# Kernel tuning notes

Measured on AMD Instinct MI355X. Metric: run time of the kernel, lower is better.

The kernel has to match this reference:

```python
import jax, jax.numpy as jnp
import numpy as np

K = 3
PAD = (K - 1) // 2


def _conv1d(x, w, b):
    # x: [B, T, C]; w: [F, C, K] (torch OIH layout); conv over T, 'same' padding
    y = jax.lax.conv_general_dilated(x.transpose(0, 2, 1), w, (1,), [(PAD, PAD)],
                                     dimension_numbers=('NCH', 'OIH', 'NCH'))
    return (y + b[None, :, None]).transpose(0, 2, 1)


def _ln(x, g, b, eps=1e-5):
    m = x.mean(-1, keepdims=True)
    v = ((x - m) ** 2).mean(-1, keepdims=True)
    return (x - m) * jax.lax.rsqrt(v + eps) * g + b


def _predictor(x, p):
    # Conv1d -> ReLU -> LN -> Conv1d -> ReLU -> LN -> Linear(F,1) -> ReLU -> squeeze
    w1, b1, g1, be1, w2, b2, g2, be2, wl, bl = p
    h = _ln(jax.nn.relu(_conv1d(x, w1, b1)), g1, be1)
    h = _ln(jax.nn.relu(_conv1d(h, w2, b2)), g2, be2)
    return jax.nn.relu(jnp.einsum('btf,f->bt', h, wl) + bl)  # [B, T]


def _length_regulate(x, dur, max_len):
    # Gather-based frame expansion: frame t comes from token i = searchsorted(cumsum(dur), t, 'right')
    cs = jnp.cumsum(dur, axis=1)                       # [B, T]
    t = jnp.arange(max_len)                            # [M]
    idx = jax.vmap(lambda c: jnp.searchsorted(c, t, side='right'))(cs)  # [B, M]
    valid = t[None, :] < cs[:, -1:]                    # [B, M]
    idx = jnp.minimum(idx, x.shape[1] - 1)
    out = jnp.take_along_axis(x, idx[:, :, None], axis=1)  # [B, M, C]
    out = jnp.where(valid[:, :, None], out, jnp.zeros((), x.dtype))
    mel_len = jnp.minimum(cs[:, -1], max_len)
    return out, mel_len


def _bucketize(x, boundaries):
    # torch.bucketize(right=False): first boundary > x  ==  searchsorted(side='right')
    return jnp.searchsorted(boundaries, x, side='right')


def setup_inputs() -> dict:
    key = jax.random.key(0)
    ks = jax.random.split(key, 12)
    B, T, M, C, F, NB = 32, 256, 2048, 256, 256, 256
    inp = {}
    inp['inputs'] = jax.random.normal(ks[0], (B, T, C), jnp.float32)
    inp['true_duration'] = jax.random.randint(ks[1], (B, T), 0, 16)
    inp['true_pitch'] = jax.random.uniform(ks[2], (B, M), jnp.float32) * 300.0
    inp['true_energy'] = jax.random.uniform(ks[3], (B, M), jnp.float32) * 200.0
    inp['mel_max_len'] = M
    inp['pitch_q'] = jnp.linspace(0.0, 300.0, NB - 1)
    inp['energy_q'] = jnp.linspace(0.0, 200.0, NB - 1)

    def pred_params(k, cin):
        kk = jax.random.split(k, 3)
        return [0.02 * jax.random.normal(kk[0], (F, cin, K)), jnp.zeros((F,)),
                jnp.ones((F,)), jnp.zeros((F,)),
                0.02 * jax.random.normal(kk[1], (F, F, K)), jnp.zeros((F,)),
                jnp.ones((F,)), jnp.zeros((F,)),
                0.02 * jax.random.normal(kk[2], (F,)), jnp.zeros(())]

    names = ['w1', 'b1', 'g1', 'be1', 'w2', 'b2', 'g2', 'be2', 'wl', 'bl']
    for i, pre in enumerate(['dp', 'pp', 'ep']):
        for n, v in zip(names, pred_params(ks[4 + i], C)):
            inp[pre + '_' + n] = v
    inp['pitch_emb'] = 0.02 * jax.random.normal(ks[8], (NB, C))
    inp['energy_emb'] = 0.02 * jax.random.normal(ks[9], (NB, C))
    return inp


def reference(inputs, true_duration, true_pitch, true_energy, mel_max_len,
              pitch_q, energy_q,
              dp_w1, dp_b1, dp_g1, dp_be1, dp_w2, dp_b2, dp_g2, dp_be2, dp_wl, dp_bl,
              pp_w1, pp_b1, pp_g1, pp_be1, pp_w2, pp_b2, pp_g2, pp_be2, pp_wl, pp_bl,
              ep_w1, ep_b1, ep_g1, ep_be1, ep_w2, ep_b2, ep_g2, ep_be2, ep_wl, ep_bl,
              pitch_emb, energy_emb):
    # Training path: expansion uses true_duration, embeddings use true pitch/energy.
    dp = (dp_w1, dp_b1, dp_g1, dp_be1, dp_w2, dp_b2, dp_g2, dp_be2, dp_wl, dp_bl)
    pp = (pp_w1, pp_b1, pp_g1, pp_be1, pp_w2, pp_b2, pp_g2, pp_be2, pp_wl, pp_bl)
    ep = (ep_w1, ep_b1, ep_g1, ep_be1, ep_w2, ep_b2, ep_g2, ep_be2, ep_wl, ep_bl)
    durations = _predictor(inputs, dp)                       # [B, T], alpha=1.0
    outputs, mel_len = _length_regulate(inputs, true_duration, mel_max_len)  # [B, M, C]
    pitches = _predictor(outputs, pp)                        # [B, M]
    outputs = outputs + pitch_emb[_bucketize(true_pitch, pitch_q)]
    energies = _predictor(outputs, ep)                       # [B, M]
    outputs = outputs + energy_emb[_bucketize(true_energy, energy_q)]
    return outputs, durations, pitches, energies, mel_len
```

## Files before the change

### kernel.cpp

```cpp
#include <hip/hip_runtime.h>
#include <hip/hip_bf16.h>
#include <stdint.h>

#define DUR_OFF 16777216
#define PIT_OFF 16785408
#define ENE_OFF 16850944
#define MEL_OFF 16916480

typedef __attribute__((ext_vector_type(8))) short short8;
typedef __attribute__((ext_vector_type(4))) float f32x4;

__device__ __forceinline__ void async16(const void* g, void* l) {
  __builtin_amdgcn_global_load_lds((__attribute__((address_space(1))) void*)g,
                                   (__attribute__((address_space(3))) void*)l, 16, 0, 0);
}

__device__ __forceinline__ unsigned short bfu(float f) {
  __hip_bfloat16 h = __float2bfloat16(f);
  return __builtin_bit_cast(unsigned short, h);
}
__device__ __forceinline__ float f_from_bf(unsigned short u) {
  return __builtin_bit_cast(float, (unsigned)u << 16);
}

__global__ void zero2_kernel(__hip_bfloat16* __restrict__ xb, __hip_bfloat16* __restrict__ h1,
                             __hip_bfloat16* __restrict__ M1, __hip_bfloat16* __restrict__ M2) {
  int buf = blockIdx.x >> 6, sub = blockIdx.x & 63;
  int b = sub >> 1, top = sub & 1;
  __hip_bfloat16* p; int L;
  if (buf == 0) { p = xb; L = 256; }
  else if (buf == 1) { p = h1; L = 256; }
  else if (buf == 2) { p = M1; L = 2048; }
  else { p = M2; L = 2048; }
  size_t row = (size_t)b * (L + 2) + (top ? (L + 1) : 0);
  p[row * 256 + threadIdx.x] = __float2bfloat16(0.0f);
}

__global__ void packfrag_kernel(const float* __restrict__ w0, const float* __restrict__ w1,
                                const float* __restrict__ w2, const float* __restrict__ w3,
                                const float* __restrict__ w4, const float* __restrict__ w5,
                                __hip_bfloat16* __restrict__ wpbase) {
  int t = blockIdx.x * 256 + threadIdx.x;
  int wsel = t / 24576;
  int rem = t % 24576;
  const float* w = wsel == 0 ? w0 : wsel == 1 ? w1 : wsel == 2 ? w2
                 : wsel == 3 ? w3 : wsel == 4 ? w4 : w5;
  __hip_bfloat16* wp = wpbase + (size_t)wsel * 196608;
  int L = rem & 63;
  int ks = (rem >> 6) & 7;
  int q = rem >> 9;
  int tap = q % 3, r = q / 3;
  int ni = r & 3, fb = r >> 2;
  int f = fb * 64 + ni * 16 + (L & 15);
  int cb = ks * 32 + ((L >> 4) << 3);
  short8 o;
#pragma unroll
  for (int e = 0; e < 8; ++e)
    o[e] = (short)bfu(w[((size_t)f * 256 + cb + e) * 3 + tap]);
  *(short8*)(wp + (size_t)rem * 8) = o;
}

__global__ void cvt_pad_kernel(const float* __restrict__ x, __hip_bfloat16* __restrict__ xb) {
  int idx = blockIdx.x * 256 + threadIdx.x;
  float4 v = ((const float4*)x)[idx];
  int c4 = idx & 63;
  int rowi = idx >> 6;
  int b = rowi >> 8, t = rowi & 255;
  ushort4 o;
  o.x = bfu(v.x); o.y = bfu(v.y); o.z = bfu(v.z); o.w = bfu(v.w);
  ((ushort4*)(xb + ((size_t)b * 258 + t + 1) * 256))[c4] = o;
}

__global__ void gather_kernel(const __hip_bfloat16* __restrict__ xb, const int* __restrict__ dur,
                              __hip_bfloat16* __restrict__ outB, float* __restrict__ mel) {
  __shared__ int scs[256];
  __shared__ int sidx[64];
  __shared__ int sval[64];
  int bch = blockIdx.x >> 5;
  int m0 = (blockIdx.x & 31) << 6;
  int tid = threadIdx.x;
  scs[tid] = dur[bch * 256 + tid];
  __syncthreads();
  for (int off = 1; off < 256; off <<= 1) {
    int add = (tid >= off) ? scs[tid - off] : 0;
    __syncthreads();
    scs[tid] += add;
    __syncthreads();
  }
  int total = scs[255];
  if (tid == 0 && (blockIdx.x & 31) == 0)
    mel[bch] = (float)(total < 2048 ? total : 2048);
  if (tid < 64) {
    int m = m0 + tid;
    int lo = 0, hi = 256;
    while (lo < hi) { int mid = (lo + hi) >> 1; if (scs[mid] <= m) lo = mid + 1; else hi = mid; }
    sidx[tid] = lo < 255 ? lo : 255;
    sval[tid] = (m < total);
  }
  __syncthreads();
  int lane = tid & 63, rs = tid >> 6;
  for (int r = rs; r < 64; r += 4) {
    ushort4 o = make_ushort4(0, 0, 0, 0);
    if (sval[r])
      o = ((const ushort4*)(xb + ((size_t)bch * 258 + sidx[r] + 1) * 256))[lane];
    ((ushort4*)(outB + ((size_t)bch * 2050 + m0 + r + 1) * 256))[lane] = o;
  }
}

__global__ void addemb_kernel(const float* __restrict__ tp, const float* __restrict__ te,
                              const float* __restrict__ pq, const float* __restrict__ eq,
                              const float* __restrict__ pemb, const float* __restrict__ eemb,
                              const __hip_bfloat16* __restrict__ M1, __hip_bfloat16* __restrict__ M2,
                              float* __restrict__ out) {
  __shared__ float sp[255], se[255];
  __shared__ int sip[64], sie[64];
  int bch = blockIdx.x >> 5;
  int m0 = (blockIdx.x & 31) << 6;
  int tid = threadIdx.x;
  if (tid < 255) { sp[tid] = pq[tid]; se[tid] = eq[tid]; }
  __syncthreads();
  if (tid < 64) {
    float xv = tp[bch * 2048 + m0 + tid];
    int lo = 0, hi = 255;
    while (lo < hi) { int mid = (lo + hi) >> 1; if (sp[mid] <= xv) lo = mid + 1; else hi = mid; }
    sip[tid] = lo;
    float ev = te[bch * 2048 + m0 + tid];
    lo = 0; hi = 255;
    while (lo < hi) { int mid = (lo + hi) >> 1; if (se[mid] <= ev) lo = mid + 1; else hi = mid; }
    sie[tid] = lo;
  }
  __syncthreads();
  int lane = tid & 63, rs = tid >> 6;
  for (int r = rs; r < 64; r += 4) {
    ushort4 mv = ((const ushort4*)(M1 + ((size_t)bch * 2050 + m0 + r + 1) * 256))[lane];
    float4 ep = ((const float4*)(pemb + (size_t)sip[r] * 256))[lane];
    float4 ee = ((const float4*)(eemb + (size_t)sie[r] * 256))[lane];
    float4 v;
    v.x = f_from_bf(mv.x) + ep.x; v.y = f_from_bf(mv.y) + ep.y;
    v.z = f_from_bf(mv.z) + ep.z; v.w = f_from_bf(mv.w) + ep.w;
    ushort4 o;
    o.x = bfu(v.x); o.y = bfu(v.y); o.z = bfu(v.z); o.w = bfu(v.w);
    ((ushort4*)(M2 + ((size_t)bch * 2050 + m0 + r + 1) * 256))[lane] = o;
    float4 w;
    w.x = v.x + ee.x; w.y = v.y + ee.y; w.z = v.z + ee.z; w.w = v.w + ee.w;
    ((float4*)(out + ((size_t)bch * 2048 + m0 + r) * 256))[lane] = w;
  }
}

__device__ __forceinline__ void loadB4(const char* Wb, int s, short8 (&dst)[4]) {
  int tap = s >> 3, ks = s & 7;
#pragma unroll
  for (int ni = 0; ni < 4; ++ni)
    dst[ni] = *(const short8*)(Wb + ((((ni * 3 + tap) << 3) + ks) << 10));
}

template <int MI>
__device__ __forceinline__ void sliceMFMA(int s, const char* lA, int rlane, int colp,
                                          const short8 (&bv)[4], f32x4 (&acc)[MI][4]) {
  const int tap = s >> 3, ks = s & 7;
  const int xorv = ((tap + rlane) & 7) << 4;
  short8 av[MI];
#pragma unroll
  for (int mi = 0; mi < MI; ++mi) {
    int a = (tap + (mi << 4) + rlane) * 512 + (ks << 6) + colp;
    av[mi] = *(const short8*)(lA + (a ^ xorv));
  }
#pragma unroll
  for (int mi = 0; mi < MI; ++mi)
#pragma unroll
    for (int ni = 0; ni < 4; ++ni)
      acc[mi][ni] = __builtin_amdgcn_mfma_f32_16x16x32_bf16(av[mi], bv[ni], acc[mi][ni], 0, 0, 0);
}

template <int EPI, int TM>
__global__ __launch_bounds__(256, 3)
void pred_gemm(const __hip_bfloat16* __restrict__ Ap, const __hip_bfloat16* __restrict__ Wf,
               const float* __restrict__ bias, const float* __restrict__ gamma,
               const float* __restrict__ beta, const float* __restrict__ wl,
               const float* __restrict__ blp, __hip_bfloat16* __restrict__ Hout,
               float* __restrict__ Sout, int L) {
  constexpr int MI = TM / 16;
  constexpr int ABYTES = (TM + 2) * 512;
  __shared__ char lA[ABYTES];
  __shared__ float lred[TM * 8];
  __shared__ float lstat[TM * 2];

  const int tid = threadIdx.x;
  const int wid = tid >> 6;
  const int lane = tid & 63;
  const int wn = wid;
  const int tiles = L / TM;
  const int b = blockIdx.x / tiles;
  const int t0 = (blockIdx.x % tiles) * TM;

  const char* Asrc = (const char*)(Ap + ((size_t)b * (L + 2) + t0) * 256);
#pragma unroll
  for (int j = 0; j < (ABYTES + 4095) / 4096; ++j) {
    int off = j * 4096 + tid * 16;
    if (off < ABYTES) {
      int so = off ^ (((off >> 9) & 7) << 4);
      async16(Asrc + so, lA + off);
    }
  }

  const char* Wb = (const char*)Wf + (size_t)wn * 98304 + lane * 16;

  f32x4 acc[MI][4];
  const f32x4 zero4 = {0.f, 0.f, 0.f, 0.f};
#pragma unroll
  for (int i = 0; i < MI; ++i)
#pragma unroll
    for (int j = 0; j < 4; ++j) acc[i][j] = zero4;

  short8 pA[4], pB[4];
  loadB4(Wb, 0, pA);

  __syncthreads();

  const int rlane = lane & 15;
  const int colp = (lane >> 4) << 4;
#pragma unroll 1
  for (int s2 = 0; s2 < 12; ++s2) {
    loadB4(Wb, 2 * s2 + 1, pB);
    sliceMFMA<MI>(2 * s2, lA, rlane, colp, pA, acc);
    if (s2 < 11) loadB4(Wb, 2 * s2 + 2, pA);
    sliceMFMA<MI>(2 * s2 + 1, lA, rlane, colp, pB, acc);
  }

  const int cb0 = (wn << 6) + rlane;
  float bi[4], gg[4], bb[4];
#pragma unroll
  for (int ni = 0; ni < 4; ++ni) {
    int col = cb0 + (ni << 4);
    bi[ni] = bias[col]; gg[ni] = gamma[col]; bb[ni] = beta[col];
  }
  const int rbase = (lane >> 4) << 2;
#pragma unroll
  for (int mi = 0; mi < MI; ++mi) {
#pragma unroll
    for (int j = 0; j < 4; ++j) {
      float s = 0.f, s2 = 0.f;
#pragma unroll
      for (int ni = 0; ni < 4; ++ni) {
        float r = fmaxf(acc[mi][ni][j] + bi[ni], 0.f);
        s += r; s2 += r * r;
      }
#pragma unroll
      for (int d = 1; d < 16; d <<= 1) { s += __shfl_xor(s, d); s2 += __shfl_xor(s2, d); }
      if ((lane & 15) == 0) {
        int row = (mi << 4) + rbase + j;
        lred[row * 8 + wn] = s;
        lred[row * 8 + 4 + wn] = s2;
      }
    }
  }
  __syncthreads();
  if (tid < TM) {
    float s = lred[tid * 8] + lred[tid * 8 + 1] + lred[tid * 8 + 2] + lred[tid * 8 + 3];
    float s2 = lred[tid * 8 + 4] + lred[tid * 8 + 5] + lred[tid * 8 + 6] + lred[tid * 8 + 7];
    float mean = s * (1.f / 256.f);
    float var = fmaxf(s2 * (1.f / 256.f) - mean * mean, 0.f);
    lstat[tid * 2] = mean;
    lstat[tid * 2 + 1] = rsqrtf(var + 1e-5f);
  }
  __syncthreads();

  if constexpr (EPI == 0) {
#pragma unroll
    for (int mi = 0; mi < MI; ++mi) {
#pragma unroll
      for (int j = 0; j < 4; ++j) {
        int row = (mi << 4) + rbase + j;
        float mean = lstat[row * 2], rstd = lstat[row * 2 + 1];
        __hip_bfloat16* hp = Hout + ((size_t)b * (L + 2) + t0 + row + 1) * 256 + cb0;
#pragma unroll
        for (int ni = 0; ni < 4; ++ni) {
          float r = fmaxf(acc[mi][ni][j] + bi[ni], 0.f);
          hp[ni << 4] = __float2bfloat16((r - mean) * rstd * gg[ni] + bb[ni]);
        }
      }
    }
  } else {
    float wlv[4];
#pragma unroll
    for (int ni = 0; ni < 4; ++ni) wlv[ni] = wl[cb0 + (ni << 4)];
#pragma unroll
    for (int mi = 0; mi < MI; ++mi) {
#pragma unroll
      for (int j = 0; j < 4; ++j) {
        int row = (mi << 4) + rbase + j;
        float mean = lstat[row * 2], rstd = lstat[row * 2 + 1];
        float ds = 0.f;
#pragma unroll
        for (int ni = 0; ni < 4; ++ni) {
          float r = fmaxf(acc[mi][ni][j] + bi[ni], 0.f);
          ds += ((r - mean) * rstd * gg[ni] + bb[ni]) * wlv[ni];
        }
#pragma unroll
        for (int d = 1; d < 16; d <<= 1) ds += __shfl_xor(ds, d);
        if ((lane & 15) == 0) lred[row * 8 + wn] = ds;
      }
    }
    __syncthreads();
    if (tid < TM) {
      float z = lred[tid * 8] + lred[tid * 8 + 1] + lred[tid * 8 + 2] + lred[tid * 8 + 3] + blp[0];
      Sout[(size_t)b * L + t0 + tid] = fmaxf(z, 0.f);
    }
  }
}

extern "C" void kernel_launch(void* const* d_in, const int* in_sizes, int n_in,
                              void* d_out, int out_size, void* d_ws, size_t ws_size,
                              hipStream_t stream) {
  const float* x = (const float*)d_in[0];
  const int* dur = (const int*)d_in[1];
  const float* tp = (const float*)d_in[2];
  const float* te = (const float*)d_in[3];
  const float* pq = (const float*)d_in[5];
  const float* eq = (const float*)d_in[6];
  const float* pemb = (const float*)d_in[37];
  const float* eemb = (const float*)d_in[38];

  char* ws = (char*)d_ws;
  __hip_bfloat16* wpb = (__hip_bfloat16*)ws;
  __hip_bfloat16* wp[6];
  for (int i = 0; i < 6; ++i) wp[i] = wpb + (size_t)i * 196608;
  __hip_bfloat16* xb = (__hip_bfloat16*)(ws + 2359296);
  __hip_bfloat16* h1dp = (__hip_bfloat16*)(ws + 6586368);
  __hip_bfloat16* M1 = (__hip_bfloat16*)(ws + 10813440);
  __hip_bfloat16* M2 = (__hip_bfloat16*)(ws + 44400640);

  float* out = (float*)d_out;

  zero2_kernel<<<256, 256, 0, stream>>>(xb, h1dp, M1, M2);
  packfrag_kernel<<<576, 256, 0, stream>>>((const float*)d_in[7], (const float*)d_in[11],
                                           (const float*)d_in[17], (const float*)d_in[21],
                                           (const float*)d_in[27], (const float*)d_in[31], wpb);
  cvt_pad_kernel<<<2048, 256, 0, stream>>>(x, xb);

  pred_gemm<0, 32><<<256, 256, 0, stream>>>(xb, wp[0], (const float*)d_in[8],
                                            (const float*)d_in[9], (const float*)d_in[10],
                                            nullptr, nullptr, h1dp, nullptr, 256);
  pred_gemm<1, 32><<<256, 256, 0, stream>>>(h1dp, wp[1], (const float*)d_in[12],
                                            (const float*)d_in[13], (const float*)d_in[14],
                                            (const float*)d_in[15], (const float*)d_in[16],
                                            nullptr, out + DUR_OFF, 256);

  gather_kernel<<<1024, 256, 0, stream>>>(xb, dur, M1, out + MEL_OFF);

  pred_gemm<0, 64><<<1024, 256, 0, stream>>>(M1, wp[2], (const float*)d_in[18],
                                             (const float*)d_in[19], (const float*)d_in[20],
                                             nullptr, nullptr, M2, nullptr, 2048);
  pred_gemm<1, 64><<<1024, 256, 0, stream>>>(M2, wp[3], (const float*)d_in[22],
                                             (const float*)d_in[23], (const float*)d_in[24],
                                             (const float*)d_in[25], (const float*)d_in[26],
                                             nullptr, out + PIT_OFF, 2048);

  addemb_kernel<<<1024, 256, 0, stream>>>(tp, te, pq, eq, pemb, eemb, M1, M2, out);

  pred_gemm<0, 64><<<1024, 256, 0, stream>>>(M2, wp[4], (const float*)d_in[28],
                                             (const float*)d_in[29], (const float*)d_in[30],
                                             nullptr, nullptr, M1, nullptr, 2048);
  pred_gemm<1, 64><<<1024, 256, 0, stream>>>(M1, wp[5], (const float*)d_in[32],
                                             (const float*)d_in[33], (const float*)d_in[34],
                                             (const float*)d_in[35], (const float*)d_in[36],
                                             nullptr, out + ENE_OFF, 2048);
}
```

Baseline: 348.2 us.

## Fuse both predictor conv layers into one kernel with halo recompute in LDS

Replaces the two-kernel conv1 and conv2 predictor pipeline with a single kernel. It loads an 82-row input tile, computes the first conv, ReLU and LayerNorm on 66 needed rows (padded to 80), and writes that bf16 intermediate back into shared memory. The second conv then runs from LDS, so the hidden activation no longer round-trips through global memory and one launch per predictor is removed. The cost is about 25% extra first-layer MFMA work for the halo rows, more LDS per block, loss of the B-fragment double buffering, and fewer blocks for the short duration predictor.

```diff
diff --git a/kernel.cpp b/kernel.cpp
--- a/kernel.cpp
+++ b/kernel.cpp
@@ -23,14 +23,13 @@
   return __builtin_bit_cast(float, (unsigned)u << 16);
 }
 
-__global__ void zero2_kernel(__hip_bfloat16* __restrict__ xb, __hip_bfloat16* __restrict__ h1,
-                             __hip_bfloat16* __restrict__ M1, __hip_bfloat16* __restrict__ M2) {
+__global__ void zero2_kernel(__hip_bfloat16* __restrict__ xb, __hip_bfloat16* __restrict__ M1,
+                             __hip_bfloat16* __restrict__ M2) {
   int buf = blockIdx.x >> 6, sub = blockIdx.x & 63;
   int b = sub >> 1, top = sub & 1;
   __hip_bfloat16* p; int L;
   if (buf == 0) { p = xb; L = 256; }
-  else if (buf == 1) { p = h1; L = 256; }
-  else if (buf == 2) { p = M1; L = 2048; }
+  else if (buf == 1) { p = M1; L = 2048; }
   else { p = M2; L = 2048; }
   size_t row = (size_t)b * (L + 2) + (top ? (L + 1) : 0);
   p[row * 256 + threadIdx.x] = __float2bfloat16(0.0f);
@@ -154,108 +153,100 @@
     dst[ni] = *(const short8*)(Wb + ((((ni * 3 + tap) << 3) + ks) << 10));
 }
 
-template <int MI>
-__device__ __forceinline__ void sliceMFMA(int s, const char* lA, int rlane, int colp,
-                                          const short8 (&bv)[4], f32x4 (&acc)[MI][4]) {
-  const int tap = s >> 3, ks = s & 7;
-  const int xorv = ((tap + rlane) & 7) << 4;
-  short8 av[MI];
-#pragma unroll
-  for (int mi = 0; mi < MI; ++mi) {
-    int a = (tap + (mi << 4) + rlane) * 512 + (ks << 6) + colp;
-    av[mi] = *(const short8*)(lA + (a ^ xorv));
-  }
-#pragma unroll
-  for (int mi = 0; mi < MI; ++mi)
-#pragma unroll
-    for (int ni = 0; ni < 4; ++ni)
-      acc[mi][ni] = __builtin_amdgcn_mfma_f32_16x16x32_bf16(av[mi], bv[ni], acc[mi][ni], 0, 0, 0);
-}
-
-template <int EPI, int TM>
 __global__ __launch_bounds__(256, 3)
-void pred_gemm(const __hip_bfloat16* __restrict__ Ap, const __hip_bfloat16* __restrict__ Wf,
-               const float* __restrict__ bias, const float* __restrict__ gamma,
-               const float* __restrict__ beta, const float* __restrict__ wl,
-               const float* __restrict__ blp, __hip_bfloat16* __restrict__ Hout,
-               float* __restrict__ Sout, int L) {
-  constexpr int MI = TM / 16;
-  constexpr int ABYTES = (TM + 2) * 512;
-  __shared__ char lA[ABYTES];
-  __shared__ float lred[TM * 8];
-  __shared__ float lstat[TM * 2];
+void fused_pred(const __hip_bfloat16* __restrict__ Ap, const __hip_bfloat16* __restrict__ Wf1,
+                const __hip_bfloat16* __restrict__ Wf2,
+                const float* __restrict__ b1, const float* __restrict__ g1,
+                const float* __restrict__ be1,
+                const float* __restrict__ b2, const float* __restrict__ g2,
+                const float* __restrict__ be2,
+                const float* __restrict__ wl, const float* __restrict__ blp,
+                float* __restrict__ Sout, int L) {
+  __shared__ char lA[41984];
+  __shared__ float lred[80 * 8];
+  __shared__ float lstat[80 * 2];
 
   const int tid = threadIdx.x;
   const int wid = tid >> 6;
   const int lane = tid & 63;
   const int wn = wid;
-  const int tiles = L / TM;
+  const int tiles = L >> 6;
   const int b = blockIdx.x / tiles;
-  const int t0 = (blockIdx.x % tiles) * TM;
-
-  const char* Asrc = (const char*)(Ap + ((size_t)b * (L + 2) + t0) * 256);
-#pragma unroll
-  for (int j = 0; j < (ABYTES + 4095) / 4096; ++j) {
+  const int t0 = (blockIdx.x % tiles) << 6;
+  const int rlane = lane & 15;
+  const int colp = (lane >> 4) << 4;
+  const int rbase = (lane >> 4) << 2;
+  const int cb0 = (wn << 6) + rlane;
+
+  const char* Asrc = (const char*)(Ap + ((size_t)b * (L + 2) + t0) * 256) - 512;
+#pragma unroll
+  for (int j = 0; j < 11; ++j) {
     int off = j * 4096 + tid * 16;
-    if (off < ABYTES) {
+    if (off < 41984) {
       int so = off ^ (((off >> 9) & 7) << 4);
       async16(Asrc + so, lA + off);
     }
   }
 
-  const char* Wb = (const char*)Wf + (size_t)wn * 98304 + lane * 16;
-
-  f32x4 acc[MI][4];
+  const char* Wb1 = (const char*)Wf1 + (size_t)wn * 98304 + lane * 16;
+  const char* Wb2 = (const char*)Wf2 + (size_t)wn * 98304 + lane * 16;
+
+  f32x4 acc1[5][4];
   const f32x4 zero4 = {0.f, 0.f, 0.f, 0.f};
 #pragma unroll
-  for (int i = 0; i < MI; ++i)
-#pragma unroll
-    for (int j = 0; j < 4; ++j) acc[i][j] = zero4;
-
-  short8 pA[4], pB[4];
-  loadB4(Wb, 0, pA);
-
-  __syncthreads();
-
-  const int rlane = lane & 15;
-  const int colp = (lane >> 4) << 4;
+  for (int i = 0; i < 5; ++i)
+#pragma unroll
+    for (int j = 0; j < 4; ++j) acc1[i][j] = zero4;
+
+  __syncthreads();
+
 #pragma unroll 1
-  for (int s2 = 0; s2 < 12; ++s2) {
-    loadB4(Wb, 2 * s2 + 1, pB);
-    sliceMFMA<MI>(2 * s2, lA, rlane, colp, pA, acc);
-    if (s2 < 11) loadB4(Wb, 2 * s2 + 2, pA);
-    sliceMFMA<MI>(2 * s2 + 1, lA, rlane, colp, pB, acc);
-  }
-
-  const int cb0 = (wn << 6) + rlane;
-  float bi[4], gg[4], bb[4];
+  for (int s = 0; s < 24; ++s) {
+    const int tap = s >> 3, ks = s & 7;
+    short8 bv[4];
+    loadB4(Wb1, s, bv);
+    const int xorv = ((tap + rlane) & 7) << 4;
+    short8 av[5];
+#pragma unroll
+    for (int mi = 0; mi < 5; ++mi) {
+      int a = (tap + (mi << 4) + rlane) * 512 + (ks << 6) + colp;
+      av[mi] = *(const short8*)(lA + (a ^ xorv));
+    }
+#pragma unroll
+    for (int mi = 0; mi < 5; ++mi)
+#pragma unroll
+      for (int ni = 0; ni < 4; ++ni)
+        acc1[mi][ni] =
+            __builtin_amdgcn_mfma_f32_16x16x32_bf16(av[mi], bv[ni], acc1[mi][ni], 0, 0, 0);
+  }
+
+  float bi1[4], gg1[4], bb1[4];
 #pragma unroll
   for (int ni = 0; ni < 4; ++ni) {
     int col = cb0 + (ni << 4);
-    bi[ni] = bias[col]; gg[ni] = gamma[col]; bb[ni] = beta[col];
-  }
-  const int rbase = (lane >> 4) << 2;
-#pragma unroll
-  for (int mi = 0; mi < MI; ++mi) {
+    bi1[ni] = b1[col]; gg1[ni] = g1[col]; bb1[ni] = be1[col];
+  }
+#pragma unroll
+  for (int mi = 0; mi < 5; ++mi) {
 #pragma unroll
     for (int j = 0; j < 4; ++j) {
       float s = 0.f, s2 = 0.f;
 #pragma unroll
       for (int ni = 0; ni < 4; ++ni) {
-        float r = fmaxf(acc[mi][ni][j] + bi[ni], 0.f);
+        float r = fmaxf(acc1[mi][ni][j] + bi1[ni], 0.f);
         s += r; s2 += r * r;
       }
 #pragma unroll
       for (int d = 1; d < 16; d <<= 1) { s += __shfl_xor(s, d); s2 += __shfl_xor(s2, d); }
       if ((lane & 15) == 0) {
-        int row = (mi << 4) + rbase + j;
-        lred[row * 8 + wn] = s;
-        lred[row * 8 + 4 + wn] = s2;
-      }
-    }
-  }
-  __syncthreads();
-  if (tid < TM) {
+        int lr = (mi << 4) + rbase + j;
+        lred[lr * 8 + wn] = s;
+        lred[lr * 8 + 4 + wn] = s2;
+      }
+    }
+  }
+  __syncthreads();
+  if (tid < 80) {
     float s = lred[tid * 8] + lred[tid * 8 + 1] + lred[tid * 8 + 2] + lred[tid * 8 + 3];
     float s2 = lred[tid * 8 + 4] + lred[tid * 8 + 5] + lred[tid * 8 + 6] + lred[tid * 8 + 7];
     float mean = s * (1.f / 256.f);
@@ -265,47 +256,111 @@
   }
   __syncthreads();
 
-  if constexpr (EPI == 0) {
-#pragma unroll
-    for (int mi = 0; mi < MI; ++mi) {
-#pragma unroll
-      for (int j = 0; j < 4; ++j) {
-        int row = (mi << 4) + rbase + j;
-        float mean = lstat[row * 2], rstd = lstat[row * 2 + 1];
-        __hip_bfloat16* hp = Hout + ((size_t)b * (L + 2) + t0 + row + 1) * 256 + cb0;
+#pragma unroll
+  for (int mi = 0; mi < 5; ++mi) {
+#pragma unroll
+    for (int j = 0; j < 4; ++j) {
+      int lr = (mi << 4) + rbase + j;
+      if (lr < 66) {
+        int rg = t0 - 1 + lr;
+        bool dead = (rg < 0) || (rg >= L);
+        float mean = lstat[lr * 2], rstd = lstat[lr * 2 + 1];
 #pragma unroll
         for (int ni = 0; ni < 4; ++ni) {
-          float r = fmaxf(acc[mi][ni][j] + bi[ni], 0.f);
-          hp[ni << 4] = __float2bfloat16((r - mean) * rstd * gg[ni] + bb[ni]);
+          float r = fmaxf(acc1[mi][ni][j] + bi1[ni], 0.f);
+          float v = dead ? 0.f : (r - mean) * rstd * gg1[ni] + bb1[ni];
+          int byte = (lr * 512 + ((cb0 + (ni << 4)) << 1)) ^ ((lr & 7) << 4);
+          *(__hip_bfloat16*)(lA + byte) = __float2bfloat16(v);
         }
       }
     }
-  } else {
-    float wlv[4];
-#pragma unroll
-    for (int ni = 0; ni < 4; ++ni) wlv[ni] = wl[cb0 + (ni << 4)];
-#pragma unroll
-    for (int mi = 0; mi < MI; ++mi) {
-#pragma unroll
-      for (int j = 0; j < 4; ++j) {
-        int row = (mi << 4) + rbase + j;
-        float mean = lstat[row * 2], rstd = lstat[row * 2 + 1];
-        float ds = 0.f;
-#pragma unroll
-        for (int ni = 0; ni < 4; ++ni) {
-          float r = fmaxf(acc[mi][ni][j] + bi[ni], 0.f);
-          ds += ((r - mean) * rstd * gg[ni] + bb[ni]) * wlv[ni];
-        }
-#pragma unroll
-        for (int d = 1; d < 16; d <<= 1) ds += __shfl_xor(ds, d);
-        if ((lane & 15) == 0) lred[row * 8 + wn] = ds;
-      }
-    }
-    __syncthreads();
-    if (tid < TM) {
-      float z = lred[tid * 8] + lred[tid * 8 + 1] + lred[tid * 8 + 2] + lred[tid * 8 + 3] + blp[0];
-      Sout[(size_t)b * L + t0 + tid] = fmaxf(z, 0.f);
-    }
+  }
+  __syncthreads();
+
+  f32x4 acc2[4][4];
+#pragma unroll
+  for (int i = 0; i < 4; ++i)
+#pragma unroll
+    for (int j = 0; j < 4; ++j) acc2[i][j] = zero4;
+
+#pragma unroll 1
+  for (int s = 0; s < 24; ++s) {
+    const int tap = s >> 3, ks = s & 7;
+    short8 bv[4];
+    loadB4(Wb2, s, bv);
+    const int xorv = ((tap + rlane) & 7) << 4;
+    short8 av[4];
+#pragma unroll
+    for (int mi = 0; mi < 4; ++mi) {
+      int a = (tap + (mi << 4) + rlane) * 512 + (ks << 6) + colp;
+      av[mi] = *(const short8*)(lA + (a ^ xorv));
+    }
+#pragma unroll
+    for (int mi = 0; mi < 4; ++mi)
+#pragma unroll
+      for (int ni = 0; ni < 4; ++ni)
+        acc2[mi][ni] =
+            __builtin_amdgcn_mfma_f32_16x16x32_bf16(av[mi], bv[ni], acc2[mi][ni], 0, 0, 0);
+  }
+
+  float bi2[4], gg2[4], bb2[4], wlv[4];
+#pragma unroll
+  for (int ni = 0; ni < 4; ++ni) {
+    int col = cb0 + (ni << 4);
+    bi2[ni] = b2[col]; gg2[ni] = g2[col]; bb2[ni] = be2[col];
+    wlv[ni] = wl[col];
+  }
+#pragma unroll
+  for (int mi = 0; mi < 4; ++mi) {
+#pragma unroll
+    for (int j = 0; j < 4; ++j) {
+      float s = 0.f, s2 = 0.f;
+#pragma unroll
+      for (int ni = 0; ni < 4; ++ni) {
+        float r = fmaxf(acc2[mi][ni][j] + bi2[ni], 0.f);
+        s += r; s2 += r * r;
+      }
+#pragma unroll
+      for (int d = 1; d < 16; d <<= 1) { s += __shfl_xor(s, d); s2 += __shfl_xor(s2, d); }
+      if ((lane & 15) == 0) {
+        int lr = (mi << 4) + rbase + j;
+        lred[lr * 8 + wn] = s;
+        lred[lr * 8 + 4 + wn] = s2;
+      }
+    }
+  }
+  __syncthreads();
+  if (tid < 64) {
+    float s = lred[tid * 8] + lred[tid * 8 + 1] + lred[tid * 8 + 2] + lred[tid * 8 + 3];
+    float s2 = lred[tid * 8 + 4] + lred[tid * 8 + 5] + lred[tid * 8 + 6] + lred[tid * 8 + 7];
+    float mean = s * (1.f / 256.f);
+    float var = fmaxf(s2 * (1.f / 256.f) - mean * mean, 0.f);
+    lstat[tid * 2] = mean;
+    lstat[tid * 2 + 1] = rsqrtf(var + 1e-5f);
+  }
+  __syncthreads();
+
+#pragma unroll
+  for (int mi = 0; mi < 4; ++mi) {
+#pragma unroll
+    for (int j = 0; j < 4; ++j) {
+      int lr = (mi << 4) + rbase + j;
+      float mean = lstat[lr * 2], rstd = lstat[lr * 2 + 1];
+      float ds = 0.f;
+#pragma unroll
+      for (int ni = 0; ni < 4; ++ni) {
+        float r = fmaxf(acc2[mi][ni][j] + bi2[ni], 0.f);
+        ds += ((r - mean) * rstd * gg2[ni] + bb2[ni]) * wlv[ni];
+      }
+#pragma unroll
+      for (int d = 1; d < 16; d <<= 1) ds += __shfl_xor(ds, d);
+      if ((lane & 15) == 0) lred[lr * 8 + wn] = ds;
+    }
+  }
+  __syncthreads();
+  if (tid < 64) {
+    float z = lred[tid * 8] + lred[tid * 8 + 1] + lred[tid * 8 + 2] + lred[tid * 8 + 3] + blp[0];
+    Sout[(size_t)b * L + t0 + tid] = fmaxf(z, 0.f);
   }
 }
 
@@ -326,43 +381,36 @@
   __hip_bfloat16* wp[6];
   for (int i = 0; i < 6; ++i) wp[i] = wpb + (size_t)i * 196608;
   __hip_bfloat16* xb = (__hip_bfloat16*)(ws + 2359296);
-  __hip_bfloat16* h1dp = (__hip_bfloat16*)(ws + 6586368);
   __hip_bfloat16* M1 = (__hip_bfloat16*)(ws + 10813440);
   __hip_bfloat16* M2 = (__hip_bfloat16*)(ws + 44400640);
 
   float* out = (float*)d_out;
 
-  zero2_kernel<<<256, 256, 0, stream>>>(xb, h1dp, M1, M2);
+  zero2_kernel<<<192, 256, 0, stream>>>(xb, M1, M2);
   packfrag_kernel<<<576, 256, 0, stream>>>((const float*)d_in[7], (const float*)d_in[11],
                                            (const float*)d_in[17], (const float*)d_in[21],
                                            (const float*)d_in[27], (const float*)d_in[31], wpb);
   cvt_pad_kernel<<<2048, 256, 0, stream>>>(x, xb);
 
-  pred_gemm<0, 32><<<256, 256, 0, stream>>>(xb, wp[0], (const float*)d_in[8],
-                                            (const float*)d_in[9], (const float*)d_in[10],
-                                            nullptr, nullptr, h1dp, nullptr, 256);
-  pred_gemm<1, 32><<<256, 256, 0, stream>>>(h1dp, wp[1], (const float*)d_in[12],
-                                            (const float*)d_in[13], (const float*)d_in[14],
-                                            (const float*)d_in[15], (const float*)d_in[16],
-                                            nullptr, out + DUR_OFF, 256);
+  fused_pred<<<128, 256, 0, stream>>>(xb, wp[0], wp[1], (const float*)d_in[8],
+                                      (const float*)d_in[9], (const float*)d_in[10],
+                                      (const float*)d_in[12], (const float*)d_in[13],
+                                      (const float*)d_in[14], (const float*)d_in[15],
+                                      (const float*)d_in[16], out + DUR_OFF, 256);
 
   gather_kernel<<<1024, 256, 0, stream>>>(xb, dur, M1, out + MEL_OFF);
 
-  pred_gemm<0, 64><<<1024, 256, 0, stream>>>(M1, wp[2], (const float*)d_in[18],
-                                             (const float*)d_in[19], (const float*)d_in[20],
-                                             nullptr, nullptr, M2, nullptr, 2048);
-  pred_gemm<1, 64><<<1024, 256, 0, stream>>>(M2, wp[3], (const float*)d_in[22],
-                                             (const float*)d_in[23], (const float*)d_in[24],
-                                             (const float*)d_in[25], (const float*)d_in[26],
-                                             nullptr, out + PIT_OFF, 2048);
+  fused_pred<<<1024, 256, 0, stream>>>(M1, wp[2], wp[3], (const float*)d_in[18],
+                                       (const float*)d_in[19], (const float*)d_in[20],
+                                       (const float*)d_in[22], (const float*)d_in[23],
+                                       (const float*)d_in[24], (const float*)d_in[25],
+                                       (const float*)d_in[26], out + PIT_OFF, 2048);
 
   addemb_kernel<<<1024, 256, 0, stream>>>(tp, te, pq, eq, pemb, eemb, M1, M2, out);
 
-  pred_gemm<0, 64><<<1024, 256, 0, stream>>>(M2, wp[4], (const float*)d_in[28],
-                                             (const float*)d_in[29], (const float*)d_in[30],
-                                             nullptr, nullptr, M1, nullptr, 2048);
-  pred_gemm<1, 64><<<1024, 256, 0, stream>>>(M1, wp[5], (const float*)d_in[32],
-                                             (const float*)d_in[33], (const float*)d_in[34],
-                                             (const float*)d_in[35], (const float*)d_in[36],
-                                             nullptr, out + ENE_OFF, 2048);
-}
+  fused_pred<<<1024, 256, 0, stream>>>(M2, wp[4], wp[5], (const float*)d_in[28],
+                                       (const float*)d_in[29], (const float*)d_in[30],
+                                       (const float*)d_in[32], (const float*)d_in[33],
+                                       (const float*)d_in[34], (const float*)d_in[35],
+                                       (const float*)d_in[36], out + ENE_OFF, 2048);
+}
```

After: 408.5 us. 1.17x slower.
